# Kernel tuning notes

Measured on AMD Instinct MI355X. Metric: run time of the kernel, lower is better.

## Reference

```python
import jax, jax.numpy as jnp
import numpy as np

MAT_MODE = [(0, 1), (0, 2), (1, 2)]
VEC_MODE = [2, 1, 0]
AABB_LO = -1.5
INV_SIZE = 2.0 / 3.0  # 2 / (hi - lo) with aabb [-1.5, 1.5]


def _bilinear2d(plane, gx, gy):
    # plane: [C,H,W]; gx,gy: [N] in [-1,1]; align_corners=True, zero padding
    C, H, W = plane.shape
    ix = (gx + 1.0) * 0.5 * (W - 1)
    iy = (gy + 1.0) * 0.5 * (H - 1)
    x0 = jnp.floor(ix).astype(jnp.int32)
    y0 = jnp.floor(iy).astype(jnp.int32)
    x1, y1 = x0 + 1, y0 + 1
    wx1 = ix - x0
    wy1 = iy - y0
    wx0 = 1.0 - wx1
    wy0 = 1.0 - wy1

    def gather(xi, yi, w):
        valid = (xi >= 0) & (xi < W) & (yi >= 0) & (yi < H)
        xc = jnp.clip(xi, 0, W - 1)
        yc = jnp.clip(yi, 0, H - 1)
        return plane[:, yc, xc] * (w * valid)  # [C,N]

    return (gather(x0, y0, wx0 * wy0) + gather(x1, y0, wx1 * wy0)
            + gather(x0, y1, wx0 * wy1) + gather(x1, y1, wx1 * wy1))


def _linear1d(line, gz):
    # line: [C,L]; gz: [N] in [-1,1]; matches grid_sample on [C,L,1] with x=0
    C, L = line.shape
    iz = (gz + 1.0) * 0.5 * (L - 1)
    z0 = jnp.floor(iz).astype(jnp.int32)
    z1 = z0 + 1
    w1 = iz - z0
    w0 = 1.0 - w1

    def gather(zi, w):
        valid = (zi >= 0) & (zi < L)
        zc = jnp.clip(zi, 0, L - 1)
        return line[:, zc] * (w * valid)  # [C,N]

    return gather(z0, w0) + gather(z1, w1)


def setup_inputs() -> dict:
    key = jax.random.key(0)
    ks = jax.random.split(key, 9)
    N, J, C, G = 262144, 24, 16, 128
    xyz = jax.random.uniform(ks[0], (N, 3), jnp.float32) * 2.0 - 1.0
    transforms = (jnp.eye(4, dtype=jnp.float32)[None]
                  + 0.05 * jax.random.normal(ks[1], (J, 4, 4), jnp.float32))
    scale = 0.032
    planes = [scale * jax.random.normal(ks[2 + i], (J, C, G, G), jnp.float32) for i in range(3)]
    lines = [scale * jax.random.normal(ks[5 + i], (J, C, G), jnp.float32) for i in range(3)]
    return {"xyz": xyz, "transforms": transforms,
            "plane0": planes[0], "plane1": planes[1], "plane2": planes[2],
            "line0": lines[0], "line1": lines[1], "line2": lines[2]}


def reference(xyz, transforms, plane0, plane1, plane2, line0, line1, line2):
    # compute_weights: per-joint transform of homogeneous points
    N = xyz.shape[0]
    xyz_h = jnp.concatenate([xyz, jnp.ones((N, 1), xyz.dtype)], axis=-1)  # [N,4]
    pts = jnp.einsum('jab,nb->jna', transforms, xyz_h)[..., :3]           # [J,N,3]
    g = (pts - AABB_LO) * INV_SIZE - 1.0                                  # normalize_coord
    g = jax.lax.stop_gradient(g)  # torch .detach() on sampling coords

    planes = (plane0, plane1, plane2)
    lines = (line0, line1, line2)
    J = transforms.shape[0]
    sigma = jnp.zeros((J, N), xyz.dtype)
    for p in range(3):
        m0, m1 = MAT_MODE[p]
        v = VEC_MODE[p]
        pf = jax.vmap(_bilinear2d)(planes[p], g[..., m0], g[..., m1])  # [J,C,N]
        lf = jax.vmap(_linear1d)(lines[p], g[..., v])                  # [J,C,N]
        sigma = sigma + jnp.sum(pf * lf, axis=1)
    return jax.nn.relu(sigma).T  # weights [N,J]
```

## Files before the change

### kernel.cpp

```cpp
#include <hip/hip_runtime.h>
#include <hip/hip_fp16.h>

#define NPTS 262144
#define NJ   24
#define NC   16
#define NG   128
#define PSZ  (NJ*NG*NG*NC)
#define LSZ  (NJ*NG*NC)
#define NBIN 4096

typedef _Float16 h2 __attribute__((ext_vector_type(2)));
typedef _Float16 h8 __attribute__((ext_vector_type(8)));

static __device__ __forceinline__ h8 splat8(float w) {
    _Float16 h = (_Float16)w;
    return (h8){h,h,h,h,h,h,h,h};
}

#define OFF_WSP   ((size_t)0)
#define OFF_WSL   (OFF_WSP + (size_t)3*PSZ*2)
#define OFF_OUTT  (OFF_WSL + (size_t)3*LSZ*2)
#define OFF_PERM  (OFF_OUTT + (size_t)NJ*NPTS*2)
#define OFF_XYZS  (OFF_PERM + (size_t)NPTS*4)
#define OFF_HIST  (OFF_XYZS + (size_t)NPTS*16)
#define OFF_CUR   (OFF_HIST + (size_t)NBIN*4)
#define WS_NEED   (OFF_CUR + (size_t)NBIN*4)


__global__ __launch_bounds__(256) void transpose_planes_c(
    const float* __restrict__ p0, const float* __restrict__ p1,
    const float* __restrict__ p2, _Float16* __restrict__ wsP)
{
    const int p = blockIdx.z, j = blockIdx.y;
    const int x = threadIdx.x & 127;
    const int y = blockIdx.x * 2 + (threadIdx.x >> 7);
    const float* src = ((p == 0) ? p0 : (p == 1) ? p1 : p2)
                     + ((size_t)j * NC * NG + y) * NG + x;
    _Float16 v[16];
#pragma unroll
    for (int c = 0; c < NC; ++c)
        v[c] = (_Float16)src[(size_t)c * NG * NG];
    _Float16* dst = wsP + (size_t)p * PSZ + (size_t)((j * NG + y) * NG + x) * NC;
    *(h8*)dst       = (h8){v[0],v[1],v[2],v[3],v[4],v[5],v[6],v[7]};
    *(h8*)(dst + 8) = (h8){v[8],v[9],v[10],v[11],v[12],v[13],v[14],v[15]};
}

__global__ __launch_bounds__(256) void transpose_lines_h(
    const float* __restrict__ l0, const float* __restrict__ l1,
    const float* __restrict__ l2, _Float16* __restrict__ wsL)
{
    const int p = blockIdx.z;
    const int idx = blockIdx.x * 256 + threadIdx.x;
    const int c = idx & 15;
    const int z = (idx >> 4) & 127;
    const int j = idx >> 11;
    const float* src = (p == 0) ? l0 : (p == 1) ? l1 : l2;
    wsL[(size_t)p * LSZ + (size_t)(j * NG + z) * NC + c] =
        (_Float16)src[(j * NC + c) * NG + z];
}


static __device__ __forceinline__ int bin_key(float x, float y, float z) {
    const int qx = min(max((int)((x + 1.0f) * 8.0f), 0), 15);
    const int qy = min(max((int)((y + 1.0f) * 8.0f), 0), 15);
    const int qz = min(max((int)((z + 1.0f) * 8.0f), 0), 15);
    return (qx << 8) | (qy << 4) | qz;
}

__global__ __launch_bounds__(256) void hist_k(
    const float* __restrict__ xyz, int* __restrict__ hist)
{
    const int n = blockIdx.x * 256 + threadIdx.x;
    atomicAdd(&hist[bin_key(xyz[3*n], xyz[3*n+1], xyz[3*n+2])], 1);
}

__global__ __launch_bounds__(256) void scan_k(
    const int* __restrict__ hist, int* __restrict__ cursor)
{
    __shared__ int ssum[256];
    const int tid = threadIdx.x;
    int loc[16], s = 0;
#pragma unroll
    for (int k = 0; k < 16; ++k) { loc[k] = hist[tid * 16 + k]; s += loc[k]; }
    ssum[tid] = s;
    __syncthreads();
    for (int off = 1; off < 256; off <<= 1) {
        int v = (tid >= off) ? ssum[tid - off] : 0;
        __syncthreads();
        ssum[tid] += v;
        __syncthreads();
    }
    int run = (tid == 0) ? 0 : ssum[tid - 1];
#pragma unroll
    for (int k = 0; k < 16; ++k) { cursor[tid * 16 + k] = run; run += loc[k]; }
}

__global__ __launch_bounds__(256) void scatter_k(
    const float* __restrict__ xyz, int* __restrict__ cursor,
    int* __restrict__ perm, float* __restrict__ xyzS )
{
    const int n = blockIdx.x * 256 + threadIdx.x;
    const float x = xyz[3*n], y = xyz[3*n+1], z = xyz[3*n+2];
    const int pos = atomicAdd(&cursor[bin_key(x, y, z)], 1);
    perm[pos] = n;
    *(float4*)(xyzS + 4*(size_t)pos) = make_float4(x, y, z, 0.0f);
}


__global__ __launch_bounds__(256) void trisample_s_k(
    const float* __restrict__ xyzS, const float* __restrict__ Tm,
    const _Float16* __restrict__ wsP, const _Float16* __restrict__ wsL,
    _Float16* __restrict__ outT )
{
    __shared__ _Float16 sL[3 * NG * NC];

    const int sb = (blockIdx.x & 7) * (49152 >> 3) + (blockIdx.x >> 3);
    const int j  = sb >> 11;
    const int s0 = (sb & 2047) << 7;

    {
        uint4* s4 = (uint4*)sL;
#pragma unroll
        for (int k = 0; k < 3; ++k) {
            const int idx = k * 256 + threadIdx.x;
            const int p = idx >> 8, r = idx & 255;
            s4[idx] = ((const uint4*)(wsL + (size_t)p * LSZ + (size_t)j * (NG*NC)))[r];
        }
    }
    __syncthreads();

    const int s  = s0 + (threadIdx.x >> 1);
    const int hh = (threadIdx.x & 1) << 3;

    const float4 pv = *(const float4*)(xyzS + 4*(size_t)s);
    const float px = pv.x, py = pv.y, pz = pv.z;
    const float* Tj = Tm + 16*j;

    float m0[3], m1[3];
    int   c0[3], c1[3];
#pragma unroll
    for (int a = 0; a < 3; ++a) {
        const float pt = fmaf(Tj[4*a+0], px,
                          fmaf(Tj[4*a+1], py,
                           fmaf(Tj[4*a+2], pz, Tj[4*a+3])));
        const float ia = fmaf(pt, 127.0f/3.0f, 63.5f);
        const float fa = floorf(ia);
        const int   i0 = (int)fa;
        const float w1 = ia - fa;
        m0[a] = (i0 >=  0 && i0 < NG    ) ? (1.0f - w1) : 0.0f;
        m1[a] = (i0 >= -1 && i0 < NG - 1) ? w1          : 0.0f;
        c0[a] = min(max(i0,     0), NG-1);
        c1[a] = min(max(i0 + 1, 0), NG-1);
    }

    const int M0[3] = {0,0,1}, M1[3] = {1,2,2}, MV[3] = {2,1,0};

    const _Float16* pbase[3];
    int rb0[3], rb1[3], cb0[3], cb1[3];
#pragma unroll
    for (int p = 0; p < 3; ++p) {
        pbase[p] = wsP + (size_t)p * PSZ + (size_t)j * (NG*NG*NC) + hh;
        rb0[p] = c0[M1[p]] * (NG*NC);  rb1[p] = c1[M1[p]] * (NG*NC);
        cb0[p] = c0[M0[p]] * NC;       cb1[p] = c1[M0[p]] * NC;
    }

    float sigma = 0.0f;
    h8 a0 = *(const h8*)(pbase[0] + rb0[0] + cb0[0]);
    h8 a1 = *(const h8*)(pbase[0] + rb0[0] + cb1[0]);
    h8 a2 = *(const h8*)(pbase[0] + rb1[0] + cb0[0]);
    h8 a3 = *(const h8*)(pbase[0] + rb1[0] + cb1[0]);
#pragma unroll
    for (int p = 0; p < 3; ++p) {
        h8 b0, b1, b2, b3;
        if (p < 2) {
            b0 = *(const h8*)(pbase[p+1] + rb0[p+1] + cb0[p+1]);
            b1 = *(const h8*)(pbase[p+1] + rb0[p+1] + cb1[p+1]);
            b2 = *(const h8*)(pbase[p+1] + rb1[p+1] + cb0[p+1]);
            b3 = *(const h8*)(pbase[p+1] + rb1[p+1] + cb1[p+1]);
        }
        const int A = M0[p], B = M1[p], V = MV[p];
        const h8 u0 = *(const h8*)(sL + (p * NG + c0[V]) * NC + hh);
        const h8 u1 = *(const h8*)(sL + (p * NG + c1[V]) * NC + hh);

        h8 pf = a0 * splat8(m0[A] * m0[B]);
        pf += a1 * splat8(m1[A] * m0[B]);
        pf += a2 * splat8(m0[A] * m1[B]);
        pf += a3 * splat8(m1[A] * m1[B]);
        h8 lf = u0 * splat8(m0[V]);
        lf += u1 * splat8(m1[V]);

#if __has_builtin(__builtin_amdgcn_fdot2)
#pragma unroll
        for (int q = 0; q < 4; ++q) {
            const h2 va = {pf[2*q], pf[2*q+1]};
            const h2 vb = {lf[2*q], lf[2*q+1]};
            sigma = __builtin_amdgcn_fdot2(va, vb, sigma, false);
        }
#else
#pragma unroll
        for (int q = 0; q < 8; ++q)
            sigma += (float)pf[q] * (float)lf[q];
#endif
        if (p < 2) { a0 = b0; a1 = b1; a2 = b2; a3 = b3; }
    }

    sigma += __shfl_xor(sigma, 1);
    if (hh == 0)
        outT[(size_t)j * NPTS + s] = (_Float16)fmaxf(sigma, 0.0f);
}


__global__ __launch_bounds__(256) void finalize_k(
    const _Float16* __restrict__ outT, const int* __restrict__ perm,
    float* __restrict__ out)
{
    const int s = blockIdx.x * 256 + threadIdx.x;
    const int n = perm[s];
    float4 o[6];
#pragma unroll
    for (int j = 0; j < NJ; ++j)
        ((float*)o)[j] = (float)outT[(size_t)j * NPTS + s];
    float4* dst = (float4*)(out + (size_t)n * NJ);
#pragma unroll
    for (int k = 0; k < 6; ++k) dst[k] = o[k];
}


__global__ __launch_bounds__(256) void simple_trisample_k(
    const float* __restrict__ xyz, const float* __restrict__ Tm,
    const float* __restrict__ p0, const float* __restrict__ p1,
    const float* __restrict__ p2, const float* __restrict__ l0,
    const float* __restrict__ l1, const float* __restrict__ l2,
    float* __restrict__ out)
{
    const int tid = blockIdx.x * 256 + threadIdx.x;
    const int j = tid >> 18;
    const int n = tid & (NPTS - 1);
    const float x = xyz[3*n+0], y = xyz[3*n+1], z = xyz[3*n+2];
    const float* Tj = Tm + 16*j;
    float g[3];
#pragma unroll
    for (int a = 0; a < 3; ++a) {
        const float pt = Tj[4*a+0]*x + Tj[4*a+1]*y + Tj[4*a+2]*z + Tj[4*a+3];
        g[a] = (pt + 1.5f) * (2.0f/3.0f) - 1.0f;
    }
    const float* P[3] = {p0, p1, p2};
    const float* L[3] = {l0, l1, l2};
    const int M0[3] = {0,0,1}, M1[3] = {1,2,2}, MV[3] = {2,1,0};
    float sigma = 0.0f;
#pragma unroll
    for (int p = 0; p < 3; ++p) {
        const float ix = (g[M0[p]] + 1.0f) * 63.5f;
        const float iy = (g[M1[p]] + 1.0f) * 63.5f;
        const float iz = (g[MV[p]] + 1.0f) * 63.5f;
        const float fx = floorf(ix), fy = floorf(iy), fz = floorf(iz);
        const int x0 = (int)fx, y0 = (int)fy, z0 = (int)fz;
        const float wx1 = ix - fx, wy1 = iy - fy, wz1 = iz - fz;
        const float mx0 = (x0   >= 0 && x0   < NG) ? (1.0f - wx1) : 0.0f;
        const float mx1 = (x0+1 >= 0 && x0+1 < NG) ? wx1 : 0.0f;
        const float my0 = (y0   >= 0 && y0   < NG) ? (1.0f - wy1) : 0.0f;
        const float my1 = (y0+1 >= 0 && y0+1 < NG) ? wy1 : 0.0f;
        const float mz0 = (z0   >= 0 && z0   < NG) ? (1.0f - wz1) : 0.0f;
        const float mz1 = (z0+1 >= 0 && z0+1 < NG) ? wz1 : 0.0f;
        const int xc0 = min(max(x0,0),NG-1), xc1 = min(max(x0+1,0),NG-1);
        const int yc0 = min(max(y0,0),NG-1), yc1 = min(max(y0+1,0),NG-1);
        const int zc0 = min(max(z0,0),NG-1), zc1 = min(max(z0+1,0),NG-1);
        const float w00 = mx0*my0, w01 = mx1*my0, w10 = mx0*my1, w11 = mx1*my1;
        const int o00 = yc0*NG+xc0, o01 = yc0*NG+xc1, o10 = yc1*NG+xc0, o11 = yc1*NG+xc1;
        const float* pb = P[p] + (size_t)j * NC * NG * NG;
        const float* lb = L[p] + (size_t)j * NC * NG;
#pragma unroll 4
        for (int c = 0; c < NC; ++c) {
            const float* pc = pb + (size_t)c * NG * NG;
            const float pf = pc[o00]*w00 + pc[o01]*w01 + pc[o10]*w10 + pc[o11]*w11;
            const float* lc = lb + (size_t)c * NG;
            sigma += pf * (lc[zc0]*mz0 + lc[zc1]*mz1);
        }
    }
    out[(size_t)n * NJ + j] = fmaxf(sigma, 0.0f);
}


extern "C" void kernel_launch(void* const* d_in, const int* in_sizes, int n_in,
                              void* d_out, int out_size, void* d_ws, size_t ws_size,
                              hipStream_t stream) {
    const float* xyz = nullptr;
    const float* Tm  = nullptr;
    const float* P[3] = {nullptr, nullptr, nullptr};
    const float* L[3] = {nullptr, nullptr, nullptr};
    int pi = 0, li = 0;
    for (int i = 0; i < n_in; ++i) {
        const int si = in_sizes[i];
        if      (si == NPTS * 3)            xyz = (const float*)d_in[i];
        else if (si == 16 * NJ)             Tm  = (const float*)d_in[i];
        else if (si == NJ * NC * NG * NG) { if (pi < 3) P[pi++] = (const float*)d_in[i]; }
        else if (si == NJ * NC * NG)      { if (li < 3) L[li++] = (const float*)d_in[i]; }
    }
    if (!xyz || !Tm || pi != 3 || li != 3) {
        xyz = (const float*)d_in[0];  Tm = (const float*)d_in[1];
        P[0] = (const float*)d_in[2]; P[1] = (const float*)d_in[3];
        P[2] = (const float*)d_in[4];
        L[0] = (const float*)d_in[5]; L[1] = (const float*)d_in[6];
        L[2] = (const float*)d_in[7];
    }
    float* out = (float*)d_out;
    char*  ws  = (char*)d_ws;

    if (ws_size >= WS_NEED) {
        _Float16* wsP   = (_Float16*)(ws + OFF_WSP);
        _Float16* wsL   = (_Float16*)(ws + OFF_WSL);
        _Float16* outT  = (_Float16*)(ws + OFF_OUTT);
        int*      perm  = (int*)     (ws + OFF_PERM);
        float*    xyzS  = (float*)   (ws + OFF_XYZS);
        int*      hist  = (int*)     (ws + OFF_HIST);
        int*      cur   = (int*)     (ws + OFF_CUR);

        hipMemsetAsync(hist, 0, (size_t)2 * NBIN * sizeof(int), stream);
        transpose_planes_c<<<dim3(NG/2, NJ, 3), 256, 0, stream>>>(P[0], P[1], P[2], wsP);
        transpose_lines_h<<<dim3(LSZ/256, 1, 3), 256, 0, stream>>>(L[0], L[1], L[2], wsL);
        hist_k<<<NPTS/256, 256, 0, stream>>>(xyz, hist);
        scan_k<<<1, 256, 0, stream>>>(hist, cur);
        scatter_k<<<NPTS/256, 256, 0, stream>>>(xyz, cur, perm, xyzS);
        trisample_s_k<<<49152, 256, 0, stream>>>(xyzS, Tm, wsP, wsL, outT);
        finalize_k<<<NPTS/256, 256, 0, stream>>>(outT, perm, out);
    } else {
        simple_trisample_k<<<(NPTS*NJ)/256, 256, 0, stream>>>(xyz, Tm, P[0], P[1], P[2],
                                                              L[0], L[1], L[2], out);
    }
}
```

Before: 195.2 us.

## Use one thread per sample in trisample and vectorize plane transpose loads

The sampling kernel now gives each thread a whole sample with all 16 channels, instead of splitting channels across two threads joined by a shuffle. This halves the block count and removes the cross-lane reduction and the duplicated coordinate math, at the cost of more registers per thread (double-buffered plane loads of 16 h8 values). The plane transpose kernel now reads float4 along x and writes four texels per thread, to cut load instruction count. The old sampling kernel is kept but no longer launched.

```diff
diff --git a/kernel.cpp b/kernel.cpp
--- a/kernel.cpp
+++ b/kernel.cpp
@@ -27,22 +27,32 @@
 #define WS_NEED   (OFF_CUR + (size_t)NBIN*4)
 
 
-__global__ __launch_bounds__(256) void transpose_planes_c(
+__global__ __launch_bounds__(256) void transpose_planes_c4(
     const float* __restrict__ p0, const float* __restrict__ p1,
     const float* __restrict__ p2, _Float16* __restrict__ wsP)
 {
     const int p = blockIdx.z, j = blockIdx.y;
-    const int x = threadIdx.x & 127;
-    const int y = blockIdx.x * 2 + (threadIdx.x >> 7);
+    const int x = (threadIdx.x & 31) * 4;
+    const int y = blockIdx.x * 8 + (threadIdx.x >> 5);
     const float* src = ((p == 0) ? p0 : (p == 1) ? p1 : p2)
                      + ((size_t)j * NC * NG + y) * NG + x;
-    _Float16 v[16];
+    float4 v[16];
 #pragma unroll
     for (int c = 0; c < NC; ++c)
-        v[c] = (_Float16)src[(size_t)c * NG * NG];
+        v[c] = *(const float4*)(src + (size_t)c * NG * NG);
     _Float16* dst = wsP + (size_t)p * PSZ + (size_t)((j * NG + y) * NG + x) * NC;
-    *(h8*)dst       = (h8){v[0],v[1],v[2],v[3],v[4],v[5],v[6],v[7]};
-    *(h8*)(dst + 8) = (h8){v[8],v[9],v[10],v[11],v[12],v[13],v[14],v[15]};
+#pragma unroll
+    for (int xx = 0; xx < 4; ++xx) {
+        const float* vf = (const float*)v;
+        h8 lo, hi;
+#pragma unroll
+        for (int c = 0; c < 8; ++c) {
+            lo[c] = (_Float16)vf[4*c + xx];
+            hi[c] = (_Float16)vf[4*(c+8) + xx];
+        }
+        *(h8*)(dst + xx*NC)     = lo;
+        *(h8*)(dst + xx*NC + 8) = hi;
+    }
 }
 
 __global__ __launch_bounds__(256) void transpose_lines_h(
@@ -107,16 +117,16 @@
 }
 
 
-__global__ __launch_bounds__(256) void trisample_s_k(
+__global__ __launch_bounds__(256) void trisample_f_k(
     const float* __restrict__ xyzS, const float* __restrict__ Tm,
     const _Float16* __restrict__ wsP, const _Float16* __restrict__ wsL,
     _Float16* __restrict__ outT )
 {
     __shared__ _Float16 sL[3 * NG * NC];
 
-    const int sb = (blockIdx.x & 7) * (49152 >> 3) + (blockIdx.x >> 3);
-    const int j  = sb >> 11;
-    const int s0 = (sb & 2047) << 7;
+    const int sb = (blockIdx.x & 7) * 3072 + (blockIdx.x >> 3);
+    const int j  = sb >> 10;
+    const int s0 = (sb & 1023) << 8;
 
     {
         uint4* s4 = (uint4*)sL;
@@ -129,9 +139,7 @@
     }
     __syncthreads();
 
-    const int s  = s0 + (threadIdx.x >> 1);
-    const int hh = (threadIdx.x & 1) << 3;
-
+    const int s = s0 + threadIdx.x;
     const float4 pv = *(const float4*)(xyzS + 4*(size_t)s);
     const float px = pv.x, py = pv.y, pz = pv.z;
     const float* Tj = Tm + 16*j;
@@ -156,6 +164,120 @@
     const int M0[3] = {0,0,1}, M1[3] = {1,2,2}, MV[3] = {2,1,0};
 
     const _Float16* pbase[3];
+    int o00[3], o01[3], o10[3], o11[3];
+#pragma unroll
+    for (int p = 0; p < 3; ++p) {
+        pbase[p] = wsP + (size_t)p * PSZ + (size_t)j * (NG*NG*NC);
+        const int r0 = c0[M1[p]] * (NG*NC), r1 = c1[M1[p]] * (NG*NC);
+        const int q0 = c0[M0[p]] * NC,      q1 = c1[M0[p]] * NC;
+        o00[p] = r0 + q0; o01[p] = r0 + q1; o10[p] = r1 + q0; o11[p] = r1 + q1;
+    }
+
+#define LOADP(dst, p) \
+    dst##00a = *(const h8*)(pbase[p] + o00[p]);     \
+    dst##00b = *(const h8*)(pbase[p] + o00[p] + 8); \
+    dst##01a = *(const h8*)(pbase[p] + o01[p]);     \
+    dst##01b = *(const h8*)(pbase[p] + o01[p] + 8); \
+    dst##10a = *(const h8*)(pbase[p] + o10[p]);     \
+    dst##10b = *(const h8*)(pbase[p] + o10[p] + 8); \
+    dst##11a = *(const h8*)(pbase[p] + o11[p]);     \
+    dst##11b = *(const h8*)(pbase[p] + o11[p] + 8);
+
+    h8 A00a,A00b,A01a,A01b,A10a,A10b,A11a,A11b;
+    h8 B00a,B00b,B01a,B01b,B10a,B10b,B11a,B11b;
+    LOADP(A, 0)
+
+    float sigA = 0.0f, sigB = 0.0f;
+#pragma unroll
+    for (int p = 0; p < 3; ++p) {
+        if (p < 2) { LOADP(B, p+1) }
+
+        const int A_ = M0[p], B_ = M1[p], V = MV[p];
+        const _Float16* lp = sL + p * (NG*NC);
+        const h8 u0a = *(const h8*)(lp + c0[V]*NC);
+        const h8 u0b = *(const h8*)(lp + c0[V]*NC + 8);
+        const h8 u1a = *(const h8*)(lp + c1[V]*NC);
+        const h8 u1b = *(const h8*)(lp + c1[V]*NC + 8);
+
+        const h8 w00 = splat8(m0[A_]*m0[B_]), w01 = splat8(m1[A_]*m0[B_]);
+        const h8 w10 = splat8(m0[A_]*m1[B_]), w11 = splat8(m1[A_]*m1[B_]);
+        const h8 z0  = splat8(m0[V]),         z1  = splat8(m1[V]);
+
+        h8 t0a = A00a * w00; t0a += A01a * w01;
+        h8 t1a = A10a * w10; t1a += A11a * w11;
+        const h8 pfa = t0a + t1a;
+        h8 t0b = A00b * w00; t0b += A01b * w01;
+        h8 t1b = A10b * w10; t1b += A11b * w11;
+        const h8 pfb = t0b + t1b;
+        h8 lfa = u0a * z0; lfa += u1a * z1;
+        h8 lfb = u0b * z0; lfb += u1b * z1;
+
+#if __has_builtin(__builtin_amdgcn_fdot2)
+#pragma unroll
+        for (int q = 0; q < 4; ++q) {
+            sigA = __builtin_amdgcn_fdot2((h2){pfa[2*q], pfa[2*q+1]},
+                                          (h2){lfa[2*q], lfa[2*q+1]}, sigA, false);
+            sigB = __builtin_amdgcn_fdot2((h2){pfb[2*q], pfb[2*q+1]},
+                                          (h2){lfb[2*q], lfb[2*q+1]}, sigB, false);
+        }
+#else
+#pragma unroll
+        for (int q = 0; q < 8; ++q) {
+            sigA += (float)pfa[q]*(float)lfa[q];
+            sigB += (float)pfb[q]*(float)lfb[q];
+        }
+#endif
+        if (p < 2) {
+            A00a=B00a; A00b=B00b; A01a=B01a; A01b=B01b;
+            A10a=B10a; A10b=B10b; A11a=B11a; A11b=B11b;
+        }
+    }
+#undef LOADP
+
+    outT[(size_t)j * NPTS + s] = (_Float16)fmaxf(sigA + sigB, 0.0f);
+}
+
+
+__global__ __launch_bounds__(256) void trisample_s_k(
+    const float* __restrict__ xyzS, const float* __restrict__ Tm,
+    const _Float16* __restrict__ wsP, const _Float16* __restrict__ wsL,
+    _Float16* __restrict__ outT)
+{
+    __shared__ _Float16 sL[3 * NG * NC];
+    const int sb = (blockIdx.x & 7) * (49152 >> 3) + (blockIdx.x >> 3);
+    const int j  = sb >> 11;
+    const int s0 = (sb & 2047) << 7;
+    {
+        uint4* s4 = (uint4*)sL;
+#pragma unroll
+        for (int k = 0; k < 3; ++k) {
+            const int idx = k * 256 + threadIdx.x;
+            const int p = idx >> 8, r = idx & 255;
+            s4[idx] = ((const uint4*)(wsL + (size_t)p * LSZ + (size_t)j * (NG*NC)))[r];
+        }
+    }
+    __syncthreads();
+    const int s  = s0 + (threadIdx.x >> 1);
+    const int hh = (threadIdx.x & 1) << 3;
+    const float4 pv = *(const float4*)(xyzS + 4*(size_t)s);
+    const float px = pv.x, py = pv.y, pz = pv.z;
+    const float* Tj = Tm + 16*j;
+    float m0[3], m1[3];
+    int   c0[3], c1[3];
+#pragma unroll
+    for (int a = 0; a < 3; ++a) {
+        const float pt = fmaf(Tj[4*a+0], px, fmaf(Tj[4*a+1], py, fmaf(Tj[4*a+2], pz, Tj[4*a+3])));
+        const float ia = fmaf(pt, 127.0f/3.0f, 63.5f);
+        const float fa = floorf(ia);
+        const int   i0 = (int)fa;
+        const float w1 = ia - fa;
+        m0[a] = (i0 >=  0 && i0 < NG    ) ? (1.0f - w1) : 0.0f;
+        m1[a] = (i0 >= -1 && i0 < NG - 1) ? w1          : 0.0f;
+        c0[a] = min(max(i0, 0), NG-1);
+        c1[a] = min(max(i0 + 1, 0), NG-1);
+    }
+    const int M0[3] = {0,0,1}, M1[3] = {1,2,2}, MV[3] = {2,1,0};
+    const _Float16* pbase[3];
     int rb0[3], rb1[3], cb0[3], cb1[3];
 #pragma unroll
     for (int p = 0; p < 3; ++p) {
@@ -163,7 +285,6 @@
         rb0[p] = c0[M1[p]] * (NG*NC);  rb1[p] = c1[M1[p]] * (NG*NC);
         cb0[p] = c0[M0[p]] * NC;       cb1[p] = c1[M0[p]] * NC;
     }
-
     float sigma = 0.0f;
     h8 a0 = *(const h8*)(pbase[0] + rb0[0] + cb0[0]);
     h8 a1 = *(const h8*)(pbase[0] + rb0[0] + cb1[0]);
@@ -181,32 +302,26 @@
         const int A = M0[p], B = M1[p], V = MV[p];
         const h8 u0 = *(const h8*)(sL + (p * NG + c0[V]) * NC + hh);
         const h8 u1 = *(const h8*)(sL + (p * NG + c1[V]) * NC + hh);
-
         h8 pf = a0 * splat8(m0[A] * m0[B]);
         pf += a1 * splat8(m1[A] * m0[B]);
         pf += a2 * splat8(m0[A] * m1[B]);
         pf += a3 * splat8(m1[A] * m1[B]);
         h8 lf = u0 * splat8(m0[V]);
         lf += u1 * splat8(m1[V]);
-
 #if __has_builtin(__builtin_amdgcn_fdot2)
 #pragma unroll
         for (int q = 0; q < 4; ++q) {
-            const h2 va = {pf[2*q], pf[2*q+1]};
-            const h2 vb = {lf[2*q], lf[2*q+1]};
-            sigma = __builtin_amdgcn_fdot2(va, vb, sigma, false);
+            sigma = __builtin_amdgcn_fdot2((h2){pf[2*q], pf[2*q+1]},
+                                           (h2){lf[2*q], lf[2*q+1]}, sigma, false);
         }
 #else
 #pragma unroll
-        for (int q = 0; q < 8; ++q)
-            sigma += (float)pf[q] * (float)lf[q];
+        for (int q = 0; q < 8; ++q) sigma += (float)pf[q] * (float)lf[q];
 #endif
         if (p < 2) { a0 = b0; a1 = b1; a2 = b2; a3 = b3; }
     }
-
     sigma += __shfl_xor(sigma, 1);
-    if (hh == 0)
-        outT[(size_t)j * NPTS + s] = (_Float16)fmaxf(sigma, 0.0f);
+    if (hh == 0) outT[(size_t)j * NPTS + s] = (_Float16)fmaxf(sigma, 0.0f);
 }
 
 
@@ -316,12 +431,12 @@
         int*      cur   = (int*)     (ws + OFF_CUR);
 
         hipMemsetAsync(hist, 0, (size_t)2 * NBIN * sizeof(int), stream);
-        transpose_planes_c<<<dim3(NG/2, NJ, 3), 256, 0, stream>>>(P[0], P[1], P[2], wsP);
+        transpose_planes_c4<<<dim3(NG/8, NJ, 3), 256, 0, stream>>>(P[0], P[1], P[2], wsP);
         transpose_lines_h<<<dim3(LSZ/256, 1, 3), 256, 0, stream>>>(L[0], L[1], L[2], wsL);
         hist_k<<<NPTS/256, 256, 0, stream>>>(xyz, hist);
         scan_k<<<1, 256, 0, stream>>>(hist, cur);
         scatter_k<<<NPTS/256, 256, 0, stream>>>(xyz, cur, perm, xyzS);
-        trisample_s_k<<<49152, 256, 0, stream>>>(xyzS, Tm, wsP, wsL, outT);
+        trisample_f_k<<<24576, 256, 0, stream>>>(xyzS, Tm, wsP, wsL, outT);
         finalize_k<<<NPTS/256, 256, 0, stream>>>(outT, perm, out);
     } else {
         simple_trisample_k<<<(NPTS*NJ)/256, 256, 0, stream>>>(xyz, Tm, P[0], P[1], P[2],
```

After: 245.4 us. 25.7% more time.
